# Kernel tuning notes

Measured on AMD Instinct MI355X. Metric: run time of the kernel, lower is better.

## Reference

```python
import jax, jax.numpy as jnp
import numpy as np

H, W, C_IN, C_OUT, N = 512, 512, 256, 256, 65536


def setup_inputs() -> dict:
    key = jax.random.key(0)
    k1, k2, k3, k4 = jax.random.split(key, 4)
    feature = jax.random.normal(k1, (1, C_IN, H, W), dtype=jnp.float32)
    weight = jax.random.normal(k2, (C_OUT, C_IN, 3, 3), dtype=jnp.float32) * 0.05
    # base sparse locations in the unpadded map; build 3x3 neighborhood indices
    # into the PADDED ([H+2, W+2]) map, exactly like F.pad + fancy indexing.
    base_h = jax.random.randint(k3, (N,), 0, H, dtype=jnp.int32)
    base_w = jax.random.randint(k4, (N,), 0, W, dtype=jnp.int32)
    dh = jnp.repeat(jnp.arange(3, dtype=jnp.int32), 3)  # [9]: 0,0,0,1,1,1,2,2,2
    dw = jnp.tile(jnp.arange(3, dtype=jnp.int32), 3)    # [9]: 0,1,2,0,1,2,...
    h_idx = base_h[None, :] + dh[:, None]  # [9, N], values in [0, H+1]
    w_idx = base_w[None, :] + dw[:, None]  # [9, N], values in [0, W+1]
    return {"feature": feature, "weight": weight, "h_idx": h_idx, "w_idx": w_idx}


def reference(feature, weight, h_idx, w_idx):
    # feature: [1, C, H, W]; weight: [Cout, C, 3, 3]; h_idx/w_idx: [9, N]
    C = feature.shape[1]
    out_ch = weight.shape[0]
    # F.pad(feature, [1,1,1,1])[0] -> [C, H+2, W+2]
    padded = jnp.pad(feature, ((0, 0), (0, 0), (1, 1), (1, 1)))[0]
    # gather 3x3 neighborhoods at sparse locations -> [C, 9, N]
    gathered = padded[:, h_idx, w_idx]
    # .view(9*C, -1): contiguous reshape gives row index c*9 + k
    g = gathered.reshape(C * 9, -1)  # [C*9, N]
    # kernel_d2s = weight.view(out, -1): row ordering c*9 + (kh*3+kw) matches
    k2d = weight.reshape(out_ch, -1)  # [Cout, C*9]
    return k2d @ g  # [Cout, N]
```

## Files before the change

kernel.cpp:

```cpp
#include <hip/hip_runtime.h>
#include <hip/hip_bf16.h>

#define HH 512
#define WW 512
#define CIN 256
#define COUT 256
#define NPTS 65536
#define PW 514
#define NPIX (PW * PW)
#define NKT 36

typedef __bf16 bf16x8 __attribute__((ext_vector_type(8)));
typedef float f32x4 __attribute__((ext_vector_type(4)));
typedef unsigned short us8 __attribute__((ext_vector_type(8)));

static __device__ __forceinline__ unsigned short f2bf(float f) {
  unsigned u = __builtin_bit_cast(unsigned, f);
  unsigned r = u + 0x7fffu + ((u >> 16) & 1u);
  return (unsigned short)(r >> 16);
}

static __device__ __forceinline__ void gload16(const void* g, void* l) {
  __builtin_amdgcn_global_load_lds(
      (const __attribute__((address_space(1))) unsigned int*)g,
      (__attribute__((address_space(3))) unsigned int*)l, 16, 0, 0);
}

__global__ __launch_bounds__(256) void prep_weight(const float* __restrict__ w,
                                                   unsigned short* __restrict__ A) {
  int i = blockIdx.x * 256 + threadIdx.x;
  int kb = i >> 14;
  int s  = (i >> 13) & 1;
  int o  = i & 8191;
  int r  = o >> 5;
  int cp = (o >> 3) & 3;
  int j  = o & 7;
  int c  = cp ^ ((r >> 1) & 3);
  int k  = kb * 64 + s * 32 + c * 8 + j;
  int t  = k >> 8;
  int ci = k & 255;
  A[i] = f2bf(w[r * 2304 + ci * 9 + t]);
}

__global__ __launch_bounds__(256) void border_zero(unsigned short* __restrict__ Ft) {
  int g = blockIdx.x * 256 + threadIdx.x;
  if (g >= 2052 * 32) return;
  int p = g >> 5, c = g & 31;
  int py, px;
  if (p < 514)        { py = 0;        px = p; }
  else if (p < 1028)  { py = 513;      px = p - 514; }
  else if (p < 1540)  { py = p - 1027; px = 0; }
  else                { py = p - 1539; px = 513; }
  *(us8*)&Ft[((size_t)py * PW + px) * 256 + c * 8] = (us8){0, 0, 0, 0, 0, 0, 0, 0};
}

__global__ __launch_bounds__(256) void transpose_feat(const float* __restrict__ f,
                                                      unsigned short* __restrict__ Ft) {
  __shared__ unsigned short lds[64 * 264];
  int pix0 = blockIdx.x * 64;
  int y = pix0 >> 9, x0 = pix0 & 511;
  int tid = threadIdx.x;
  int p = tid & 63;
  int cb = tid >> 6;
  const float* src = f + pix0 + p;
  for (int c8 = 0; c8 < 8; ++c8) {
    us8 v;
#pragma unroll
    for (int j = 0; j < 8; ++j) {
      int ci = cb * 64 + c8 * 8 + j;
      v[j] = f2bf(src[ci * 262144]);
    }
    *(us8*)&lds[p * 264 + cb * 64 + c8 * 8] = v;
  }
  __syncthreads();
  int cic = tid & 31;
  int pr = tid >> 5;
  for (int g = 0; g < 8; ++g) {
    int p2 = pr + g * 8;
    us8 v = *(const us8*)&lds[p2 * 264 + cic * 8];
    *(us8*)&Ft[((size_t)((y + 1) * PW + x0 + 1 + p2)) * 256 + cic * 8] = v;
  }
}

__global__ __launch_bounds__(512, 2) void gemm_gather(
    const unsigned short* __restrict__ A,
    const unsigned short* __restrict__ Ft,
    const int* __restrict__ hidx,
    const int* __restrict__ widx,
    float* __restrict__ out) {
  __shared__ unsigned short lds[65536];
  unsigned short* ldsB = lds + 32768;

  int tid = threadIdx.x;
  int lane = tid & 63, wv = tid >> 6;
  int wm = wv & 1, wn = wv >> 1;
  int n0 = blockIdx.x << 8;

  int c0 = tid >> 2;
  int cc = (tid & 3) ^ ((tid >> 3) & 3);
  long pixA = (long)hidx[n0 + c0] * PW + widx[n0 + c0];
  long pixB = (long)hidx[n0 + 128 + c0] * PW + widx[n0 + 128 + c0];
  const unsigned short* FtB0 = Ft + pixA * 256 + cc * 8;
  const unsigned short* FtB1 = Ft + pixB * 256 + cc * 8;

#define STAGE_A(dbuf, kb_, s_)                                                \
  do {                                                                        \
    const unsigned short* g_ = A + (kb_) * 16384 + (s_) * 8192 + tid * 8;     \
    unsigned short* l_ = lds + (dbuf) * 16384 + (s_) * 8192 + tid * 8;        \
    gload16(g_, l_);                                                          \
    gload16(g_ + 4096, l_ + 4096);                                            \
  } while (0)

#define STAGE_B(dbuf, s_, base_)                                              \
  do {                                                                        \
    unsigned short* l_ = ldsB + (dbuf) * 16384 + (s_) * 8192 + tid * 8;       \
    gload16(FtB0 + (base_) + (s_) * 32, l_);                                  \
    gload16(FtB1 + (base_) + (s_) * 32, l_ + 4096);                           \
  } while (0)

#define LDA(dst, dbuf, s_, mi_)                                               \
  do {                                                                        \
    int r_ = wm * 128 + (mi_) * 16 + (lane & 15);                             \
    int cp_ = (lane >> 4) ^ ((r_ >> 1) & 3);                                  \
    dst = *(const bf16x8*)&lds[(dbuf) * 16384 + (s_) * 8192 + r_ * 32 + cp_ * 8]; \
  } while (0)

#define LDB(dst, dbuf, s_, nj_)                                               \
  do {                                                                        \
    int col_ = wn * 64 + (nj_) * 16 + (lane & 15);                            \
    int cp_ = (lane >> 4) ^ ((col_ >> 1) & 3);                                \
    dst = *(const bf16x8*)&ldsB[(dbuf) * 16384 + (s_) * 8192 + col_ * 32 + cp_ * 8]; \
  } while (0)

#define MFMA16(mq_)                                                           \
  do {                                                                        \
    __builtin_amdgcn_s_setprio(1);                                            \
    _Pragma("unroll") for (int mi = 0; mi < 4; ++mi)                          \
        _Pragma("unroll") for (int nj = 0; nj < 4; ++nj)                      \
            acc[(mq_) * 4 + mi][nj] = __builtin_amdgcn_mfma_f32_16x16x32_bf16( \
                af[mi], bfr[nj], acc[(mq_) * 4 + mi][nj], 0, 0, 0);           \
    __builtin_amdgcn_s_setprio(0);                                            \
  } while (0)

  f32x4 acc[8][4];
#pragma unroll
  for (int mi = 0; mi < 8; ++mi)
#pragma unroll
    for (int nj = 0; nj < 4; ++nj)
      acc[mi][nj] = (f32x4){0.f, 0.f, 0.f, 0.f};

  STAGE_A(0, 0, 0);
  STAGE_B(0, 0, 0);
  STAGE_A(0, 0, 1);
  STAGE_B(0, 1, 0);
  asm volatile("s_waitcnt vmcnt(4)" ::: "memory");
  __builtin_amdgcn_s_barrier();

  for (int kb = 0; kb < NKT - 1; ++kb) {
    int d = kb & 1;
    int kn = kb + 1;
    int tp = kn >> 2;
    int q3 = tp / 3;
    int dtb = (q3 * PW + (tp - q3 * 3)) * 256 + (kn & 3) * 64;

    bf16x8 af[4], bfr[4];
    LDA(af[0], d, 0, 0); LDA(af[1], d, 0, 1); LDA(af[2], d, 0, 2); LDA(af[3], d, 0, 3);
    LDB(bfr[0], d, 0, 0); LDB(bfr[1], d, 0, 1); LDB(bfr[2], d, 0, 2); LDB(bfr[3], d, 0, 3);
    STAGE_A(d ^ 1, kn, 0);
    __builtin_amdgcn_s_barrier();
    MFMA16(0);
    __builtin_amdgcn_s_barrier();
    LDA(af[0], d, 0, 4); LDA(af[1], d, 0, 5); LDA(af[2], d, 0, 6); LDA(af[3], d, 0, 7);
    STAGE_B(d ^ 1, 0, dtb);
    __builtin_amdgcn_s_barrier();
    MFMA16(1);
    asm volatile("s_waitcnt vmcnt(4)" ::: "memory");
    __builtin_amdgcn_s_barrier();
    LDA(af[0], d, 1, 0); LDA(af[1], d, 1, 1); LDA(af[2], d, 1, 2); LDA(af[3], d, 1, 3);
    LDB(bfr[0], d, 1, 0); LDB(bfr[1], d, 1, 1); LDB(bfr[2], d, 1, 2); LDB(bfr[3], d, 1, 3);
    STAGE_A(d ^ 1, kn, 1);
    __builtin_amdgcn_s_barrier();
    MFMA16(0);
    __builtin_amdgcn_s_barrier();
    LDA(af[0], d, 1, 4); LDA(af[1], d, 1, 5); LDA(af[2], d, 1, 6); LDA(af[3], d, 1, 7);
    STAGE_B(d ^ 1, 1, dtb);
    __builtin_amdgcn_s_barrier();
    MFMA16(1);
    asm volatile("s_waitcnt vmcnt(4)" ::: "memory");
    __builtin_amdgcn_s_barrier();
  }

  {
    const int d = (NKT - 1) & 1;
    bf16x8 af[4], bfr[4];
    LDA(af[0], d, 0, 0); LDA(af[1], d, 0, 1); LDA(af[2], d, 0, 2); LDA(af[3], d, 0, 3);
    LDB(bfr[0], d, 0, 0); LDB(bfr[1], d, 0, 1); LDB(bfr[2], d, 0, 2); LDB(bfr[3], d, 0, 3);
    __builtin_amdgcn_s_barrier();
    MFMA16(0);
    __builtin_amdgcn_s_barrier();
    LDA(af[0], d, 0, 4); LDA(af[1], d, 0, 5); LDA(af[2], d, 0, 6); LDA(af[3], d, 0, 7);
    __builtin_amdgcn_s_barrier();
    MFMA16(1);
    asm volatile("s_waitcnt vmcnt(0)" ::: "memory");
    __builtin_amdgcn_s_barrier();
    LDA(af[0], d, 1, 0); LDA(af[1], d, 1, 1); LDA(af[2], d, 1, 2); LDA(af[3], d, 1, 3);
    LDB(bfr[0], d, 1, 0); LDB(bfr[1], d, 1, 1); LDB(bfr[2], d, 1, 2); LDB(bfr[3], d, 1, 3);
    __builtin_amdgcn_s_barrier();
    MFMA16(0);
    __builtin_amdgcn_s_barrier();
    LDA(af[0], d, 1, 4); LDA(af[1], d, 1, 5); LDA(af[2], d, 1, 6); LDA(af[3], d, 1, 7);
    __builtin_amdgcn_s_barrier();
    MFMA16(1);
  }

  int ocol = n0 + wn * 64 + (lane & 15);
  int r0 = (lane >> 4) * 4;
#pragma unroll
  for (int mi = 0; mi < 8; ++mi)
#pragma unroll
    for (int nj = 0; nj < 4; ++nj)
#pragma unroll
      for (int r = 0; r < 4; ++r)
        out[(size_t)(wm * 128 + mi * 16 + r0 + r) * NPTS + ocol + nj * 16] = acc[mi][nj][r];

#undef STAGE_A
#undef STAGE_B
#undef LDA
#undef LDB
#undef MFMA16
}

__global__ __launch_bounds__(256) void naive_conv(const float* __restrict__ f,
                                                  const float* __restrict__ w,
                                                  const int* __restrict__ hi,
                                                  const int* __restrict__ wi,
                                                  float* __restrict__ out) {
  int idx = blockIdx.x * 256 + threadIdx.x;
  int n = idx & (NPTS - 1);
  int co = idx >> 16;
  int bh = hi[n] - 1;
  int bw = wi[n] - 1;
  float acc = 0.f;
  for (int ci = 0; ci < CIN; ++ci) {
    const float* fc = f + (size_t)ci * 262144;
    const float* wc = w + (size_t)co * 2304 + ci * 9;
#pragma unroll
    for (int t = 0; t < 9; ++t) {
      int y = bh + t / 3, x = bw + t % 3;
      float v = (y >= 0 && y < 512 && x >= 0 && x < 512) ? fc[y * 512 + x] : 0.f;
      acc += wc[t] * v;
    }
  }
  out[(size_t)co * NPTS + n] = acc;
}

extern "C" void kernel_launch(void* const* d_in, const int* in_sizes, int n_in,
                              void* d_out, int out_size, void* d_ws, size_t ws_size,
                              hipStream_t stream) {
  const float* feature = (const float*)d_in[0];
  const float* weight  = (const float*)d_in[1];
  const int* hidx      = (const int*)d_in[2];
  const int* widx      = (const int*)d_in[3];
  float* out           = (float*)d_out;

  const size_t FT_OFF = 2ull * 1024 * 1024;
  const size_t FT_BYTES = (size_t)NPIX * 256 * 2;
  const size_t NEED = FT_OFF + FT_BYTES;

  if (ws_size >= NEED) {
    unsigned short* Abf = (unsigned short*)d_ws;
    unsigned short* Ft = (unsigned short*)((char*)d_ws + FT_OFF);
    prep_weight<<<(NKT * 16384) / 256, 256, 0, stream>>>(weight, Abf);
    border_zero<<<(2052 * 32 + 255) / 256, 256, 0, stream>>>(Ft);
    transpose_feat<<<262144 / 64, 256, 0, stream>>>(feature, Ft);
    gemm_gather<<<NPTS / 256, 512, 0, stream>>>(Abf, Ft, hidx, widx, out);
  } else {
    naive_conv<<<(COUT * NPTS) / 256, 256, 0, stream>>>(feature, weight, hidx, widx, out);
  }
}
```

Before: 176.0 us.

## Switch gather-GEMM to 32x32x16 MFMA with 4-stage K=32 pipeline

Replaces the 16x16x32 MFMA tiling with 32x32x16 bf16 MFMAs (4x2 tiles per wave) and shrinks the K step from 64 to 32. The double buffer becomes a four-slot LDS ring that prefetches three tiles ahead, with adjusted vmcnt waits. The weight prep layout and the epilogue row mapping change to match. The intent is fewer LDS fragment reads per FLOP and deeper latency hiding for the gathered loads. The cost is more barriers per unit of K and a reworked output write pattern.

```diff
diff --git a/kernel.cpp b/kernel.cpp
--- a/kernel.cpp
+++ b/kernel.cpp
@@ -8,10 +8,10 @@
 #define NPTS 65536
 #define PW 514
 #define NPIX (PW * PW)
-#define NKT 36
+#define NKT 72
 
 typedef __bf16 bf16x8 __attribute__((ext_vector_type(8)));
-typedef float f32x4 __attribute__((ext_vector_type(4)));
+typedef float f32x16 __attribute__((ext_vector_type(16)));
 typedef unsigned short us8 __attribute__((ext_vector_type(8)));
 
 static __device__ __forceinline__ unsigned short f2bf(float f) {
@@ -29,14 +29,13 @@
 __global__ __launch_bounds__(256) void prep_weight(const float* __restrict__ w,
                                                    unsigned short* __restrict__ A) {
   int i = blockIdx.x * 256 + threadIdx.x;
-  int kb = i >> 14;
-  int s  = (i >> 13) & 1;
+  int kt = i >> 13;
   int o  = i & 8191;
   int r  = o >> 5;
   int cp = (o >> 3) & 3;
   int j  = o & 7;
   int c  = cp ^ ((r >> 1) & 3);
-  int k  = kb * 64 + s * 32 + c * 8 + j;
+  int k  = kt * 32 + c * 8 + j;
   int t  = k >> 8;
   int ci = k & 255;
   A[i] = f2bf(w[r * 2304 + ci * 9 + t]);
@@ -103,131 +102,112 @@
   const unsigned short* FtB0 = Ft + pixA * 256 + cc * 8;
   const unsigned short* FtB1 = Ft + pixB * 256 + cc * 8;
 
-#define STAGE_A(dbuf, kb_, s_)                                                \
-  do {                                                                        \
-    const unsigned short* g_ = A + (kb_) * 16384 + (s_) * 8192 + tid * 8;     \
-    unsigned short* l_ = lds + (dbuf) * 16384 + (s_) * 8192 + tid * 8;        \
+#define STAGE_A(kt_)                                                          \
+  do {                                                                        \
+    const unsigned short* g_ = A + (size_t)(kt_) * 8192 + tid * 8;            \
+    unsigned short* l_ = lds + ((kt_) & 3) * 8192 + tid * 8;                  \
     gload16(g_, l_);                                                          \
     gload16(g_ + 4096, l_ + 4096);                                            \
   } while (0)
 
-#define STAGE_B(dbuf, s_, base_)                                              \
-  do {                                                                        \
-    unsigned short* l_ = ldsB + (dbuf) * 16384 + (s_) * 8192 + tid * 8;       \
-    gload16(FtB0 + (base_) + (s_) * 32, l_);                                  \
-    gload16(FtB1 + (base_) + (s_) * 32, l_ + 4096);                           \
-  } while (0)
-
-#define LDA(dst, dbuf, s_, mi_)                                               \
-  do {                                                                        \
-    int r_ = wm * 128 + (mi_) * 16 + (lane & 15);                             \
-    int cp_ = (lane >> 4) ^ ((r_ >> 1) & 3);                                  \
-    dst = *(const bf16x8*)&lds[(dbuf) * 16384 + (s_) * 8192 + r_ * 32 + cp_ * 8]; \
-  } while (0)
-
-#define LDB(dst, dbuf, s_, nj_)                                               \
-  do {                                                                        \
-    int col_ = wn * 64 + (nj_) * 16 + (lane & 15);                            \
-    int cp_ = (lane >> 4) ^ ((col_ >> 1) & 3);                                \
-    dst = *(const bf16x8*)&ldsB[(dbuf) * 16384 + (s_) * 8192 + col_ * 32 + cp_ * 8]; \
-  } while (0)
-
-#define MFMA16(mq_)                                                           \
+#define STAGE_B(kt_)                                                          \
+  do {                                                                        \
+    int tp_ = (kt_) >> 3;                                                     \
+    int q_ = tp_ / 3;                                                         \
+    long off_ = (long)(q_ * PW + (tp_ - q_ * 3)) * 256 + ((kt_) & 7) * 32;    \
+    unsigned short* l_ = ldsB + ((kt_) & 3) * 8192 + tid * 8;                 \
+    gload16(FtB0 + off_, l_);                                                 \
+    gload16(FtB1 + off_, l_ + 4096);                                          \
+  } while (0)
+
+#define LDA(dst, buf_, kg_, mt_)                                              \
+  do {                                                                        \
+    int r_ = wm * 128 + (mt_) * 32 + (lane & 31);                             \
+    int c_ = ((kg_) * 2 + (lane >> 5)) ^ ((r_ >> 1) & 3);                     \
+    dst = *(const bf16x8*)&lds[(buf_) * 8192 + r_ * 32 + c_ * 8];             \
+  } while (0)
+
+#define LDB(dst, buf_, kg_, nt_)                                              \
+  do {                                                                        \
+    int col_ = wn * 64 + (nt_) * 32 + (lane & 31);                            \
+    int c_ = ((kg_) * 2 + (lane >> 5)) ^ ((col_ >> 1) & 3);                   \
+    dst = *(const bf16x8*)&ldsB[(buf_) * 8192 + col_ * 32 + c_ * 8];          \
+  } while (0)
+
+#define MFMA8()                                                               \
   do {                                                                        \
     __builtin_amdgcn_s_setprio(1);                                            \
-    _Pragma("unroll") for (int mi = 0; mi < 4; ++mi)                          \
-        _Pragma("unroll") for (int nj = 0; nj < 4; ++nj)                      \
-            acc[(mq_) * 4 + mi][nj] = __builtin_amdgcn_mfma_f32_16x16x32_bf16( \
-                af[mi], bfr[nj], acc[(mq_) * 4 + mi][nj], 0, 0, 0);           \
+    acc[0][0] = __builtin_amdgcn_mfma_f32_32x32x16_bf16(af0, b0, acc[0][0], 0, 0, 0); \
+    acc[0][1] = __builtin_amdgcn_mfma_f32_32x32x16_bf16(af0, b1, acc[0][1], 0, 0, 0); \
+    acc[1][0] = __builtin_amdgcn_mfma_f32_32x32x16_bf16(af1, b0, acc[1][0], 0, 0, 0); \
+    acc[1][1] = __builtin_amdgcn_mfma_f32_32x32x16_bf16(af1, b1, acc[1][1], 0, 0, 0); \
+    acc[2][0] = __builtin_amdgcn_mfma_f32_32x32x16_bf16(af2, b0, acc[2][0], 0, 0, 0); \
+    acc[2][1] = __builtin_amdgcn_mfma_f32_32x32x16_bf16(af2, b1, acc[2][1], 0, 0, 0); \
+    acc[3][0] = __builtin_amdgcn_mfma_f32_32x32x16_bf16(af3, b0, acc[3][0], 0, 0, 0); \
+    acc[3][1] = __builtin_amdgcn_mfma_f32_32x32x16_bf16(af3, b1, acc[3][1], 0, 0, 0); \
     __builtin_amdgcn_s_setprio(0);                                            \
   } while (0)
 
-  f32x4 acc[8][4];
-#pragma unroll
-  for (int mi = 0; mi < 8; ++mi)
-#pragma unroll
-    for (int nj = 0; nj < 4; ++nj)
-      acc[mi][nj] = (f32x4){0.f, 0.f, 0.f, 0.f};
-
-  STAGE_A(0, 0, 0);
-  STAGE_B(0, 0, 0);
-  STAGE_A(0, 0, 1);
-  STAGE_B(0, 1, 0);
-  asm volatile("s_waitcnt vmcnt(4)" ::: "memory");
+#define TILE(kt_, DOSTAGE_, WAITN_)                                           \
+  do {                                                                        \
+    int buf_ = (kt_) & 3;                                                     \
+    bf16x8 af0, af1, af2, af3, b0, b1;                                        \
+    LDA(af0, buf_, 0, 0); LDA(af1, buf_, 0, 1);                               \
+    LDA(af2, buf_, 0, 2); LDA(af3, buf_, 0, 3);                               \
+    LDB(b0, buf_, 0, 0); LDB(b1, buf_, 0, 1);                                 \
+    if (DOSTAGE_) STAGE_A((kt_) + 3);                                         \
+    __builtin_amdgcn_s_barrier();                                             \
+    MFMA8();                                                                  \
+    __builtin_amdgcn_s_barrier();                                             \
+    LDA(af0, buf_, 1, 0); LDA(af1, buf_, 1, 1);                               \
+    LDA(af2, buf_, 1, 2); LDA(af3, buf_, 1, 3);                               \
+    LDB(b0, buf_, 1, 0); LDB(b1, buf_, 1, 1);                                 \
+    if (DOSTAGE_) STAGE_B((kt_) + 3);                                         \
+    __builtin_amdgcn_s_barrier();                                             \
+    MFMA8();                                                                  \
+    if ((WAITN_) == 8) asm volatile("s_waitcnt vmcnt(8)" ::: "memory");       \
+    else if ((WAITN_) == 4) asm volatile("s_waitcnt vmcnt(4)" ::: "memory");  \
+    else if ((WAITN_) == 0) asm volatile("s_waitcnt vmcnt(0)" ::: "memory");  \
+    __builtin_amdgcn_s_barrier();                                             \
+  } while (0)
+
+  f32x16 acc[4][2];
+#pragma unroll
+  for (int mt = 0; mt < 4; ++mt)
+#pragma unroll
+    for (int nt = 0; nt < 2; ++nt)
+      acc[mt][nt] = (f32x16)(0.f);
+
+  STAGE_A(0); STAGE_B(0);
+  STAGE_A(1); STAGE_B(1);
+  STAGE_A(2); STAGE_B(2);
+  asm volatile("s_waitcnt vmcnt(8)" ::: "memory");
   __builtin_amdgcn_s_barrier();
 
-  for (int kb = 0; kb < NKT - 1; ++kb) {
-    int d = kb & 1;
-    int kn = kb + 1;
-    int tp = kn >> 2;
-    int q3 = tp / 3;
-    int dtb = (q3 * PW + (tp - q3 * 3)) * 256 + (kn & 3) * 64;
-
-    bf16x8 af[4], bfr[4];
-    LDA(af[0], d, 0, 0); LDA(af[1], d, 0, 1); LDA(af[2], d, 0, 2); LDA(af[3], d, 0, 3);
-    LDB(bfr[0], d, 0, 0); LDB(bfr[1], d, 0, 1); LDB(bfr[2], d, 0, 2); LDB(bfr[3], d, 0, 3);
-    STAGE_A(d ^ 1, kn, 0);
-    __builtin_amdgcn_s_barrier();
-    MFMA16(0);
-    __builtin_amdgcn_s_barrier();
-    LDA(af[0], d, 0, 4); LDA(af[1], d, 0, 5); LDA(af[2], d, 0, 6); LDA(af[3], d, 0, 7);
-    STAGE_B(d ^ 1, 0, dtb);
-    __builtin_amdgcn_s_barrier();
-    MFMA16(1);
-    asm volatile("s_waitcnt vmcnt(4)" ::: "memory");
-    __builtin_amdgcn_s_barrier();
-    LDA(af[0], d, 1, 0); LDA(af[1], d, 1, 1); LDA(af[2], d, 1, 2); LDA(af[3], d, 1, 3);
-    LDB(bfr[0], d, 1, 0); LDB(bfr[1], d, 1, 1); LDB(bfr[2], d, 1, 2); LDB(bfr[3], d, 1, 3);
-    STAGE_A(d ^ 1, kn, 1);
-    __builtin_amdgcn_s_barrier();
-    MFMA16(0);
-    __builtin_amdgcn_s_barrier();
-    LDA(af[0], d, 1, 4); LDA(af[1], d, 1, 5); LDA(af[2], d, 1, 6); LDA(af[3], d, 1, 7);
-    STAGE_B(d ^ 1, 1, dtb);
-    __builtin_amdgcn_s_barrier();
-    MFMA16(1);
-    asm volatile("s_waitcnt vmcnt(4)" ::: "memory");
-    __builtin_amdgcn_s_barrier();
-  }
-
-  {
-    const int d = (NKT - 1) & 1;
-    bf16x8 af[4], bfr[4];
-    LDA(af[0], d, 0, 0); LDA(af[1], d, 0, 1); LDA(af[2], d, 0, 2); LDA(af[3], d, 0, 3);
-    LDB(bfr[0], d, 0, 0); LDB(bfr[1], d, 0, 1); LDB(bfr[2], d, 0, 2); LDB(bfr[3], d, 0, 3);
-    __builtin_amdgcn_s_barrier();
-    MFMA16(0);
-    __builtin_amdgcn_s_barrier();
-    LDA(af[0], d, 0, 4); LDA(af[1], d, 0, 5); LDA(af[2], d, 0, 6); LDA(af[3], d, 0, 7);
-    __builtin_amdgcn_s_barrier();
-    MFMA16(1);
-    asm volatile("s_waitcnt vmcnt(0)" ::: "memory");
-    __builtin_amdgcn_s_barrier();
-    LDA(af[0], d, 1, 0); LDA(af[1], d, 1, 1); LDA(af[2], d, 1, 2); LDA(af[3], d, 1, 3);
-    LDB(bfr[0], d, 1, 0); LDB(bfr[1], d, 1, 1); LDB(bfr[2], d, 1, 2); LDB(bfr[3], d, 1, 3);
-    __builtin_amdgcn_s_barrier();
-    MFMA16(0);
-    __builtin_amdgcn_s_barrier();
-    LDA(af[0], d, 1, 4); LDA(af[1], d, 1, 5); LDA(af[2], d, 1, 6); LDA(af[3], d, 1, 7);
-    __builtin_amdgcn_s_barrier();
-    MFMA16(1);
-  }
-
-  int ocol = n0 + wn * 64 + (lane & 15);
-  int r0 = (lane >> 4) * 4;
-#pragma unroll
-  for (int mi = 0; mi < 8; ++mi)
-#pragma unroll
-    for (int nj = 0; nj < 4; ++nj)
-#pragma unroll
-      for (int r = 0; r < 4; ++r)
-        out[(size_t)(wm * 128 + mi * 16 + r0 + r) * NPTS + ocol + nj * 16] = acc[mi][nj][r];
+  for (int kt = 0; kt < NKT - 3; ++kt)
+    TILE(kt, 1, 8);
+  TILE(69, 0, 4);
+  TILE(70, 0, 0);
+  TILE(71, 0, -1);
 
 #undef STAGE_A
 #undef STAGE_B
 #undef LDA
 #undef LDB
-#undef MFMA16
+#undef MFMA8
+#undef TILE
+
+  int colb = n0 + wn * 64 + (lane & 31);
+  int rb = wm * 128 + ((lane >> 5) << 2);
+#pragma unroll
+  for (int mt = 0; mt < 4; ++mt)
+#pragma unroll
+    for (int nt = 0; nt < 2; ++nt)
+#pragma unroll
+      for (int r = 0; r < 16; ++r) {
+        int row = rb + mt * 32 + (r & 3) + ((r >> 2) << 3);
+        out[(size_t)row * NPTS + colb + nt * 32] = acc[mt][nt][r];
+      }
 }
 
 __global__ __launch_bounds__(256) void naive_conv(const float* __restrict__ f,
@@ -270,7 +250,7 @@
   if (ws_size >= NEED) {
     unsigned short* Abf = (unsigned short*)d_ws;
     unsigned short* Ft = (unsigned short*)((char*)d_ws + FT_OFF);
-    prep_weight<<<(NKT * 16384) / 256, 256, 0, stream>>>(weight, Abf);
+    prep_weight<<<(NKT * 8192) / 256, 256, 0, stream>>>(weight, Abf);
     border_zero<<<(2052 * 32 + 255) / 256, 256, 0, stream>>>(Ft);
     transpose_feat<<<262144 / 64, 256, 0, stream>>>(feature, Ft);
     gemm_gather<<<NPTS / 256, 512, 0, stream>>>(Abf, Ft, hidx, widx, out);
```

Result: no change. 177.7 us (+1.0%).
